# Kernel optimization log

Hardware: AMD Instinct MI355X
Metric: run time of the kernel (lower is better)

## Reference

```python
import jax, jax.numpy as jnp
import numpy as np
import math

N_HEADS = 16
D_HEAD = 64
DEPTH = 12
LAMBDA_INIT = 0.8 - 0.6 * math.exp(-0.3 * DEPTH)
SCALING = 1.0 / math.sqrt(D_HEAD)
RMS_EPS = 1e-6
B, T = 4, 1024


def setup_inputs() -> dict:
    key = jax.random.key(0)
    ks = jax.random.split(key, 8)
    q = jax.random.normal(ks[0], (B, 2 * N_HEADS, T, D_HEAD), dtype=jnp.float32)
    k = jax.random.normal(ks[1], (B, 2 * N_HEADS, T, D_HEAD), dtype=jnp.float32)
    v = jax.random.normal(ks[2], (B, N_HEADS, T, 2 * D_HEAD), dtype=jnp.float32)
    # causal mask, broadcast over batch/heads; masked_fill where mask == 0
    mask = jnp.tril(jnp.ones((1, 1, T, T), dtype=jnp.int32))
    lambda_q1 = 0.1 * jax.random.normal(ks[3], (N_HEADS, D_HEAD), dtype=jnp.float32)
    lambda_k1 = 0.1 * jax.random.normal(ks[4], (N_HEADS, D_HEAD), dtype=jnp.float32)
    lambda_q2 = 0.1 * jax.random.normal(ks[5], (N_HEADS, D_HEAD), dtype=jnp.float32)
    lambda_k2 = 0.1 * jax.random.normal(ks[6], (N_HEADS, D_HEAD), dtype=jnp.float32)
    rms_weight = jnp.ones((2 * D_HEAD,), dtype=jnp.float32)
    return {"q": q, "k": k, "v": v, "mask": mask,
            "lambda_q1": lambda_q1, "lambda_k1": lambda_k1,
            "lambda_q2": lambda_q2, "lambda_k2": lambda_k2,
            "rms_weight": rms_weight, "flash_attn": 0}


def _rms_norm(x, weight):
    var = jnp.mean(jnp.square(x), axis=-1, keepdims=True)
    return x * jax.lax.rsqrt(var + RMS_EPS) * weight


def reference(q, k, v, mask, lambda_q1, lambda_k1, lambda_q2, lambda_k2, rms_weight, flash_attn):
    # lambda reparameterization: scalar per head
    lambda_1 = jnp.exp(jnp.sum(lambda_q1 * lambda_k1, axis=-1))  # [H]
    lambda_2 = jnp.exp(jnp.sum(lambda_q2 * lambda_k2, axis=-1))  # [H]
    lambda_final = lambda_1 - lambda_2 + LAMBDA_INIT             # [H]

    Bq, H2, Tq, Dh = q.shape
    # dual attention scores over 2*n_heads heads: [B, 2H, T, T]
    attn = jnp.einsum('bhtd,bhsd->bhts', q, k) * SCALING
    attn = jnp.where(mask == 0, -jnp.inf, attn)
    attn = jax.nn.softmax(attn.astype(jnp.float32), axis=-1).astype(q.dtype)
    # consecutive head pairs -> (attn1, attn2)
    attn = attn.reshape(Bq, H2 // 2, 2, Tq, Tq)
    attn = attn[:, :, 0] - lambda_final[None, :, None, None] * attn[:, :, 1]
    # dropout is identity in eval mode
    y = jnp.einsum('bhts,bhsd->bhtd', attn, v)  # [B, H, T, 2*d_head]
    y = _rms_norm(y, rms_weight)
    y = y * (1.0 - LAMBDA_INIT)
    return y
```

## Files before the change

kernel.cpp:

```cpp
#include <hip/hip_runtime.h>


typedef _Float16 f16x4 __attribute__((ext_vector_type(4)));
typedef _Float16 f16x8 __attribute__((ext_vector_type(8)));
typedef float    f32x4 __attribute__((ext_vector_type(4)));

constexpr int   TSEQ        = 1024;
constexpr int   DQK         = 64;
constexpr int   DVDIM       = 128;
constexpr float SCALING     = 0.125f;
constexpr float LAMBDA_INIT = 0.7836057665316245f;
constexpr float ONE_MINUS_LI= 1.0f - LAMBDA_INIT;
constexpr float RMS_EPS     = 1e-6f;
constexpr float LOG2E       = 1.4426950408889634f;
constexpr float DEFER_THR   = 8.0f;

__global__ __launch_bounds__(256, 2)
void diff_attn_kernel(const float* __restrict__ qg, const float* __restrict__ kg,
                      const float* __restrict__ vg,
                      const float* __restrict__ lq1, const float* __restrict__ lk1,
                      const float* __restrict__ lq2, const float* __restrict__ lk2,
                      const float* __restrict__ rmsw, float* __restrict__ out)
{
    __shared__ _Float16 Klds[2][64][72];
    __shared__ _Float16 Vt[128][68];

    const int hp   = blockIdx.x;
    const int a    = blockIdx.y;
    const int b    = blockIdx.z;
    const int t    = threadIdx.x;
    const int w    = t >> 6;
    const int lane = t & 63;
    const int n    = lane & 15;
    const int quad = lane >> 4;

    float a1 = lq1[hp*64 + lane] * lk1[hp*64 + lane];
    float a2 = lq2[hp*64 + lane] * lk2[hp*64 + lane];
    #pragma unroll
    for (int d = 1; d < 64; d <<= 1) { a1 += __shfl_xor(a1, d); a2 += __shfl_xor(a2, d); }
    const float lambda = __expf(a1) - __expf(a2) + LAMBDA_INIT;

    const float* kb = kg + ((size_t)(b*32 + hp*2)) * TSEQ * DQK;
    const float* vb = vg + ((size_t)(b*16 + hp))   * TSEQ * DVDIM;

    const int jj   = t & 15;
    const int sg   = t >> 4;
    const int dvb  = jj * 8;
    const int s0   = sg * 4;
    const int rotw = (jj & 7) * 8;
    const int d8   = t & 7;

    float4 kr[4][2], vr[8];

    auto load_tile = [&](int sbase) {
        #pragma unroll
        for (int i = 0; i < 4; ++i) {
            const int row = (i*256 + t) >> 3;
            const int h = row >> 6, sr = row & 63;
            const float* p = kb + ((size_t)h*TSEQ + sbase + sr)*DQK + d8*8;
            kr[i][0] = *(const float4*)p;
            kr[i][1] = *(const float4*)(p + 4);
        }
        const float* vp = vb + (size_t)(sbase + s0)*DVDIM + dvb;
        #pragma unroll
        for (int r = 0; r < 4; ++r) {
            vr[2*r]   = *(const float4*)(vp + r*DVDIM);
            vr[2*r+1] = *(const float4*)(vp + r*DVDIM + 4);
        }
    };

    auto write_tile = [&]() {
        #pragma unroll
        for (int i = 0; i < 4; ++i) {
            const int row = (i*256 + t) >> 3;
            const int h = row >> 6, sr = row & 63;
            f16x8 kk;
            kk[0]=(_Float16)kr[i][0].x; kk[1]=(_Float16)kr[i][0].y;
            kk[2]=(_Float16)kr[i][0].z; kk[3]=(_Float16)kr[i][0].w;
            kk[4]=(_Float16)kr[i][1].x; kk[5]=(_Float16)kr[i][1].y;
            kk[6]=(_Float16)kr[i][1].z; kk[7]=(_Float16)kr[i][1].w;
            *(f16x8*)&Klds[h][sr][d8*8] = kk;
        }
        float vrow[4][8];
        #pragma unroll
        for (int r = 0; r < 4; ++r) {
            vrow[r][0]=vr[2*r].x;   vrow[r][1]=vr[2*r].y;
            vrow[r][2]=vr[2*r].z;   vrow[r][3]=vr[2*r].w;
            vrow[r][4]=vr[2*r+1].x; vrow[r][5]=vr[2*r+1].y;
            vrow[r][6]=vr[2*r+1].z; vrow[r][7]=vr[2*r+1].w;
        }
        #pragma unroll
        for (int mI = 0; mI < 8; ++mI) {
            f16x4 pk;
            pk[0]=(_Float16)vrow[0][mI]; pk[1]=(_Float16)vrow[1][mI];
            pk[2]=(_Float16)vrow[2][mI]; pk[3]=(_Float16)vrow[3][mI];
            *(f16x4*)&Vt[dvb + mI][(s0 + rotw) & 63] = pk;
        }
    };

    const float qscale = SCALING * LOG2E;
    load_tile(0);

    for (int part = 0; part < 2; ++part) {
        const int qt    = part ? (15 - a) : a;
        const int qbase = qt * 64;
        const int qw0   = qbase + w * 16;
        const int qrow  = qw0 + n;
        const int nT    = qt + 1;

        f16x8 Qf[2][2];
        #pragma unroll
        for (int h = 0; h < 2; ++h) {
            const float* qp = qg + (((size_t)(b*32 + hp*2 + h)) * TSEQ + qrow) * DQK + quad*8;
            #pragma unroll
            for (int ks = 0; ks < 2; ++ks) {
                float4 x = *(const float4*)(qp + ks*32);
                float4 y = *(const float4*)(qp + ks*32 + 4);
                f16x8 f;
                f[0]=(_Float16)(x.x*qscale); f[1]=(_Float16)(x.y*qscale);
                f[2]=(_Float16)(x.z*qscale); f[3]=(_Float16)(x.w*qscale);
                f[4]=(_Float16)(y.x*qscale); f[5]=(_Float16)(y.y*qscale);
                f[6]=(_Float16)(y.z*qscale); f[7]=(_Float16)(y.w*qscale);
                Qf[h][ks] = f;
            }
        }

        f32x4 O[2][8];
        #pragma unroll
        for (int h = 0; h < 2; ++h)
            #pragma unroll
            for (int d = 0; d < 8; ++d) O[h][d] = (f32x4){0.f,0.f,0.f,0.f};
        float m_[2] = { -__builtin_huge_valf(), -__builtin_huge_valf() };
        float l_[2] = { 0.f, 0.f };

        for (int tile = 0; tile < nT; ++tile) {
            const int sbase = tile * 64;
            __syncthreads();
            write_tile();
            __syncthreads();
            if (tile + 1 < nT)      load_tile((tile + 1) * 64);
            else if (part == 0)     load_tile(0);

            const bool diag = (tile == qt);
            const int  nact = diag ? (w + 1) : 4;

            f16x4 pb[2][4];
            #pragma unroll
            for (int h = 0; h < 2; ++h) {
                f32x4 St[4];
                #pragma unroll
                for (int sub = 0; sub < 4; ++sub) {
                    if (sub < nact) {
                        f16x8 k0 = *(const f16x8*)&Klds[h][sub*16 + n][quad*8];
                        f16x8 k1 = *(const f16x8*)&Klds[h][sub*16 + n][32 + quad*8];
                        f32x4 c = (f32x4){0.f,0.f,0.f,0.f};
                        c = __builtin_amdgcn_mfma_f32_16x16x32_f16(k0, Qf[h][0], c, 0, 0, 0);
                        c = __builtin_amdgcn_mfma_f32_16x16x32_f16(k1, Qf[h][1], c, 0, 0, 0);
                        St[sub] = c;
                    }
                }
                float vals[16];
                #pragma unroll
                for (int sub = 0; sub < 4; ++sub) {
                    if (sub < nact) {
                        #pragma unroll
                        for (int r = 0; r < 4; ++r) {
                            const int s = sbase + sub*16 + quad*4 + r;
                            float x = St[sub][r];
                            if (diag && s > qrow) x = -__builtin_huge_valf();
                            vals[sub*4 + r] = x;
                        }
                    }
                }
                float mx = -__builtin_huge_valf();
                #pragma unroll
                for (int sub = 0; sub < 4; ++sub)
                    if (sub < nact)
                        #pragma unroll
                        for (int r = 0; r < 4; ++r) mx = fmaxf(mx, vals[sub*4 + r]);
                mx = fmaxf(mx, __shfl_xor(mx, 16));
                mx = fmaxf(mx, __shfl_xor(mx, 32));
                const float mold  = m_[h];
                const bool  defer = __all(mx <= mold + DEFER_THR);
                const float mnew  = defer ? mold : fmaxf(mold, mx);
                float rs = 0.f;
                #pragma unroll
                for (int sub = 0; sub < 4; ++sub) {
                    if (sub < nact) {
                        #pragma unroll
                        for (int r = 0; r < 4; ++r) {
                            const float p = exp2f(vals[sub*4 + r] - mnew);
                            rs += p;
                            pb[h][sub][r] = (_Float16)p;
                        }
                    }
                }
                rs += __shfl_xor(rs, 16);
                rs += __shfl_xor(rs, 32);
                m_[h] = mnew;
                if (defer) {
                    l_[h] += rs;
                } else {
                    const float alpha = exp2f(mold - mnew);
                    l_[h] = l_[h] * alpha + rs;
                    #pragma unroll
                    for (int d = 0; d < 8; ++d) {
                        O[h][d][0] *= alpha; O[h][d][1] *= alpha;
                        O[h][d][2] *= alpha; O[h][d][3] *= alpha;
                    }
                }
            }
            __builtin_amdgcn_s_setprio(1);
            #pragma unroll
            for (int dd = 0; dd < 8; ++dd) {
                const int rot_r = ((2*dd + (n >> 3)) & 7) * 8;
                #pragma unroll
                for (int sub = 0; sub < 4; ++sub) {
                    if (sub < nact) {
                        f16x4 va = *(const f16x4*)&Vt[dd*16 + n][(sub*16 + quad*4 + rot_r) & 63];
                        O[0][dd] = __builtin_amdgcn_mfma_f32_16x16x16f16(va, pb[0][sub], O[0][dd], 0, 0, 0);
                        O[1][dd] = __builtin_amdgcn_mfma_f32_16x16x16f16(va, pb[1][sub], O[1][dd], 0, 0, 0);
                    }
                }
            }
            __builtin_amdgcn_s_setprio(0);
        }

        const float i1 = 1.0f   / l_[0];
        const float i2 = lambda / l_[1];
        float yv[8][4];
        float ss = 0.f;
        #pragma unroll
        for (int d = 0; d < 8; ++d)
            #pragma unroll
            for (int r = 0; r < 4; ++r) {
                const float y = O[0][d][r] * i1 - O[1][d][r] * i2;
                yv[d][r] = y; ss += y * y;
            }
        ss += __shfl_xor(ss, 16);
        ss += __shfl_xor(ss, 32);
        const float sc = rsqrtf(ss * (1.0f/128.0f) + RMS_EPS) * ONE_MINUS_LI;

        float* ob = out + (((size_t)(b*16 + hp)) * TSEQ + qrow) * DVDIM;
        #pragma unroll
        for (int d = 0; d < 8; ++d) {
            const int dv = d*16 + quad*4;
            float4 wv = *(const float4*)&rmsw[dv];
            float4 o;
            o.x = yv[d][0] * sc * wv.x;
            o.y = yv[d][1] * sc * wv.y;
            o.z = yv[d][2] * sc * wv.z;
            o.w = yv[d][3] * sc * wv.w;
            *(float4*)(ob + dv) = o;
        }
    }
}

extern "C" void kernel_launch(void* const* d_in, const int* in_sizes, int n_in,
                              void* d_out, int out_size, void* d_ws, size_t ws_size,
                              hipStream_t stream) {
    const float* q    = (const float*)d_in[0];
    const float* k    = (const float*)d_in[1];
    const float* v    = (const float*)d_in[2];
    const float* lq1  = (const float*)d_in[4];
    const float* lk1  = (const float*)d_in[5];
    const float* lq2  = (const float*)d_in[6];
    const float* lk2  = (const float*)d_in[7];
    const float* rmsw = (const float*)d_in[8];
    float* out = (float*)d_out;

    dim3 grid(16, 8, 4);
    dim3 block(256);
    diff_attn_kernel<<<grid, block, 0, stream>>>(q, k, v, lq1, lk1, lq2, lk2, rmsw, out);
}
```

Before: 205.3 us.

## Double-buffer K/V LDS tiles to drop one barrier per iteration

Splits the K and transposed-V shared-memory tiles into two buffers. The next tile is written into the idle buffer while the softmax and PV MFMA work runs on the current one, and the loop now needs one __syncthreads per iteration instead of two. The global-load prefetch order is linearised across both query-tile parts through a seq_base mapping. This doubles LDS use per block, which could limit the two-blocks-per-CU occupancy, and it depends on the total tile count being exactly 17 for the j<16 guards.

```diff
diff --git a/kernel.cpp b/kernel.cpp
--- a/kernel.cpp
+++ b/kernel.cpp
@@ -22,8 +22,8 @@
                       const float* __restrict__ lq2, const float* __restrict__ lk2,
                       const float* __restrict__ rmsw, float* __restrict__ out)
 {
-    __shared__ _Float16 Klds[2][64][72];
-    __shared__ _Float16 Vt[128][68];
+    __shared__ _Float16 Klds[2][2][64][72];
+    __shared__ _Float16 Vt[2][128][68];
 
     const int hp   = blockIdx.x;
     const int a    = blockIdx.y;
@@ -69,7 +69,7 @@
         }
     };
 
-    auto write_tile = [&]() {
+    auto write_tile = [&](int bi) {
         #pragma unroll
         for (int i = 0; i < 4; ++i) {
             const int row = (i*256 + t) >> 3;
@@ -79,7 +79,7 @@
             kk[2]=(_Float16)kr[i][0].z; kk[3]=(_Float16)kr[i][0].w;
             kk[4]=(_Float16)kr[i][1].x; kk[5]=(_Float16)kr[i][1].y;
             kk[6]=(_Float16)kr[i][1].z; kk[7]=(_Float16)kr[i][1].w;
-            *(f16x8*)&Klds[h][sr][d8*8] = kk;
+            *(f16x8*)&Klds[bi][h][sr][d8*8] = kk;
         }
         float vrow[4][8];
         #pragma unroll
@@ -94,13 +94,21 @@
             f16x4 pk;
             pk[0]=(_Float16)vrow[0][mI]; pk[1]=(_Float16)vrow[1][mI];
             pk[2]=(_Float16)vrow[2][mI]; pk[3]=(_Float16)vrow[3][mI];
-            *(f16x4*)&Vt[dvb + mI][(s0 + rotw) & 63] = pk;
+            *(f16x4*)&Vt[bi][dvb + mI][(s0 + rotw) & 63] = pk;
         }
     };
 
     const float qscale = SCALING * LOG2E;
+
+    const int A = a;
+    auto seq_base = [&](int i) { return (i <= A) ? i*64 : (i - A - 1)*64; };
+
     load_tile(0);
-
+    write_tile(0);
+    __syncthreads();
+    load_tile(seq_base(1));
+
+    int j = 0;
     for (int part = 0; part < 2; ++part) {
         const int qt    = part ? (15 - a) : a;
         const int qbase = qt * 64;
@@ -133,13 +141,9 @@
         float m_[2] = { -__builtin_huge_valf(), -__builtin_huge_valf() };
         float l_[2] = { 0.f, 0.f };
 
-        for (int tile = 0; tile < nT; ++tile) {
+        for (int tile = 0; tile < nT; ++tile, ++j) {
+            const int cur   = j & 1;
             const int sbase = tile * 64;
-            __syncthreads();
-            write_tile();
-            __syncthreads();
-            if (tile + 1 < nT)      load_tile((tile + 1) * 64);
-            else if (part == 0)     load_tile(0);
 
             const bool diag = (tile == qt);
             const int  nact = diag ? (w + 1) : 4;
@@ -151,8 +155,8 @@
                 #pragma unroll
                 for (int sub = 0; sub < 4; ++sub) {
                     if (sub < nact) {
-                        f16x8 k0 = *(const f16x8*)&Klds[h][sub*16 + n][quad*8];
-                        f16x8 k1 = *(const f16x8*)&Klds[h][sub*16 + n][32 + quad*8];
+                        f16x8 k0 = *(const f16x8*)&Klds[cur][h][sub*16 + n][quad*8];
+                        f16x8 k1 = *(const f16x8*)&Klds[cur][h][sub*16 + n][32 + quad*8];
                         f32x4 c = (f32x4){0.f,0.f,0.f,0.f};
                         c = __builtin_amdgcn_mfma_f32_16x16x32_f16(k0, Qf[h][0], c, 0, 0, 0);
                         c = __builtin_amdgcn_mfma_f32_16x16x32_f16(k1, Qf[h][1], c, 0, 0, 0);
@@ -210,6 +214,12 @@
                     }
                 }
             }
+
+            if (j < 16) {
+                write_tile(cur ^ 1);
+                if (j < 15) load_tile(seq_base(j + 2));
+            }
+
             __builtin_amdgcn_s_setprio(1);
             #pragma unroll
             for (int dd = 0; dd < 8; ++dd) {
@@ -217,13 +227,15 @@
                 #pragma unroll
                 for (int sub = 0; sub < 4; ++sub) {
                     if (sub < nact) {
-                        f16x4 va = *(const f16x4*)&Vt[dd*16 + n][(sub*16 + quad*4 + rot_r) & 63];
+                        f16x4 va = *(const f16x4*)&Vt[cur][dd*16 + n][(sub*16 + quad*4 + rot_r) & 63];
                         O[0][dd] = __builtin_amdgcn_mfma_f32_16x16x16f16(va, pb[0][sub], O[0][dd], 0, 0, 0);
                         O[1][dd] = __builtin_amdgcn_mfma_f32_16x16x16f16(va, pb[1][sub], O[1][dd], 0, 0, 0);
                     }
                 }
             }
             __builtin_amdgcn_s_setprio(0);
+
+            if (j < 16) __syncthreads();
         }
 
         const float i1 = 1.0f   / l_[0];
```

After: 203.1 us. About the same (-1.1%).
